# Performance work log

Measured on AMD Instinct MI355X. Metric: run time of the kernel, lower is better.

## Reference

```python
import jax, jax.numpy as jnp
import numpy as np

EPS = 1e-10


def setup_inputs() -> dict:
    key = jax.random.key(0)
    ks = jax.random.split(key, 8)
    N, C, H, W = 32, 512, 14, 14
    D, HID = 2048, 256
    s1 = 1.0 / np.sqrt(C + D)
    s2 = 1.0 / np.sqrt(HID)
    return {
        "local_feature": jax.random.normal(ks[0], (N, C, H, W), jnp.float32),
        "global_feature": jax.random.normal(ks[1], (N, D, 1, 1), jnp.float32),
        "W1": jax.random.normal(ks[2], (C + D, HID), jnp.float32) * s1,
        "b1": jnp.zeros((HID,), jnp.float32),
        "W2": jax.random.normal(ks[3], (HID, HID), jnp.float32) * s2,
        "b2": jnp.zeros((HID,), jnp.float32),
        "W3": jax.random.normal(ks[4], (HID, 1), jnp.float32) * s2,
        "b3": jnp.zeros((1,), jnp.float32),
    }


def reference(local_feature, global_feature, W1, b1, W2, b2, W3, b3):
    # Vectorized form of DMIEstimator.calculate_mi (the per-sample Python loop
    # collapsed into one batched pass with a block-diagonal negative mask).
    N, C, H, W = local_feature.shape
    hw = H * W
    nhw = N * hw
    D = global_feature.shape[1]

    lf = jnp.transpose(local_feature, (0, 2, 3, 1)).reshape(nhw, C)   # [nhw, C]
    gf = global_feature[:, :, 0, 0]                                   # [N, D]

    # combined = cat([global, local], -1); split the first Linear accordingly
    # so the [N*nhw, C+D] concat tensor is never materialized.
    h_loc = lf @ W1[D:]                        # [nhw, HID]
    h_glb = gf @ W1[:D] + b1                   # [N, HID]
    h1 = jax.nn.relu(h_glb[:, None, :] + h_loc[None, :, :])  # [N, nhw, HID]
    h2 = jax.nn.relu(h1 @ W2 + b2)                            # [N, nhw, HID]
    scores = (h2 @ W3)[..., 0] + b3[0]                        # [N, nhw]

    mx = jnp.max(scores, axis=1, keepdims=True)               # [N, 1]
    ex = jnp.exp(scores - mx)

    # negatives for sample i exclude its own hw block [hw*i, hw*(i+1))
    own = (jnp.arange(nhw)[None, :] // hw) == jnp.arange(N)[:, None]  # [N, nhw]
    neg_mean = jnp.where(own, 0.0, ex).sum(axis=1) / (nhw - hw) + EPS  # [N]

    # positive (diagonal) block of scores: scores[i, hw*i : hw*(i+1)]
    pos = scores.reshape(N, N, hw)[jnp.arange(N), jnp.arange(N)]       # [N, hw]

    mi = pos - mx - jnp.log(neg_mean)[:, None]                         # [N, hw]
    return mi.reshape(N, H, W)
```

## Files before the change

### kernel.cpp

```cpp
#include <hip/hip_runtime.h>
#include <math.h>

#define NB   32
#define CC   512
#define DD   2048
#define HWP  196
#define NHW  6272
#define HID  256

typedef _Float16 h8 __attribute__((ext_vector_type(8)));
typedef _Float16 h4 __attribute__((ext_vector_type(4)));
typedef float    f4 __attribute__((ext_vector_type(4)));
union F4H8 { f4 f; h8 h; };

__device__ __forceinline__ int fragIdx(int j, int k) {
    return ((j >> 6) << 14) + (((k >> 5) * 4 + ((j & 63) >> 4)) << 9)
         + (((((k >> 3) & 3) << 4) + (j & 15)) << 3) + (k & 7);
}

__global__ __launch_bounds__(256) void prep_kernel(const float* __restrict__ lf,
                                                   const float* __restrict__ gf,
                                                   const float* __restrict__ W1,
                                                   const float* __restrict__ W2,
                                                   float* __restrict__ hpart,
                                                   _Float16* __restrict__ W2F,
                                                   _Float16* __restrict__ W1F,
                                                   _Float16* __restrict__ lf16T) {
    int bid = blockIdx.x, tid = threadIdx.x;
    if (bid < 512) {
        int i = bid >> 4, ky = bid & 15, k = tid;
        const float* g = gf + (size_t)i * DD + ky * 128;
        const float* w = W1 + (size_t)(ky * 128) * HID + k;
        float a0 = 0.f, a1 = 0.f, a2 = 0.f, a3 = 0.f;
        #pragma unroll 8
        for (int r = 0; r < 128; r += 4) {
            a0 = fmaf(g[r + 0], w[(size_t)(r + 0) * HID], a0);
            a1 = fmaf(g[r + 1], w[(size_t)(r + 1) * HID], a1);
            a2 = fmaf(g[r + 2], w[(size_t)(r + 2) * HID], a2);
            a3 = fmaf(g[r + 3], w[(size_t)(r + 3) * HID], a3);
        }
        hpart[((size_t)i * 16 + ky) * HID + k] = (a0 + a1) + (a2 + a3);
    } else if (bid < 608) {
        int tg = (bid - 512) * 256 + tid;
        if (tg < 8192) {
            int t = tg, F = t >> 6, l = t & 63;
            int k2t = F >> 3, ks = F & 7;
            int kb = ks * 32 + (l >> 4) * 8;
            int n  = k2t * 16 + (l & 15);
            _Float16* o = W2F + (size_t)t * 8;
            #pragma unroll
            for (int j = 0; j < 8; j++) o[j] = (_Float16)W2[(size_t)(kb + j) * HID + n];
        } else {
            int t = tg - 8192, F = t >> 6, l = t & 63;
            int k2t = F >> 4, ks = F & 15;
            int kb = ks * 32 + (l >> 4) * 8;
            int n  = k2t * 16 + (l & 15);
            const float* W1c = W1 + (size_t)DD * HID;
            _Float16* o = W1F + (size_t)t * 8;
            #pragma unroll
            for (int j = 0; j < 8; j++) o[j] = (_Float16)W1c[(size_t)(kb + j) * HID + n];
        }
    } else {
        __shared__ _Float16 sT[64][HWP + 4];
        int b = bid - 608;
        int n = b >> 3, c0 = (b & 7) * 64;
        for (int task = tid; task < 64 * 49; task += 256) {
            int c = task / 49, f = task - c * 49;
            f4 v = *(const f4*)&lf[((size_t)n * CC + c0 + c) * HWP + f * 4];
            h4 o = { (_Float16)v.x, (_Float16)v.y, (_Float16)v.z, (_Float16)v.w };
            *(h4*)&sT[c][f * 4] = o;
        }
        __syncthreads();
        for (int task = tid; task < 8 * HWP; task += 256) {
            int ch = task / HWP, p = task - ch * HWP;
            h8 o;
            #pragma unroll
            for (int cc = 0; cc < 8; cc++) o[cc] = sT[ch * 8 + cc][p];
            *(h8*)&lf16T[((size_t)(n * HWP + p)) * CC + c0 + ch * 8] = o;
        }
    }
}

__global__ __launch_bounds__(256, 2) void hlocF_kernel(const _Float16* __restrict__ lf16T,
                                                       const _Float16* __restrict__ W1F,
                                                       const float* __restrict__ hpart,
                                                       const float* __restrict__ b1,
                                                       _Float16* __restrict__ g16,
                                                       _Float16* __restrict__ hF) {
    if (blockIdx.x == 196) {
        int kh = blockIdx.y;
        for (int x = threadIdx.x; x < 16 * HID; x += 256) {
            int i = kh * 16 + (x >> 8), k = x & 255;
            float s = b1[k];
            #pragma unroll
            for (int ky = 0; ky < 16; ky++) s += hpart[((size_t)i * 16 + ky) * HID + k];
            g16[(size_t)i * HID + k] = (_Float16)s;
        }
        return;
    }
    __shared__ _Float16 sLf[32][CC + 16];
    int tid = threadIdx.x;
    int w = tid >> 6, l = tid & 63, quad = l >> 4, ln = l & 15;
    int j0 = blockIdx.x * 32;
    int khalf = blockIdx.y;

    #pragma unroll
    for (int s = 0; s < 8; s++) {
        int y = s * 256 + tid;
        int row = y >> 6, col = (y & 63) * 8;
        h8 v = *(const h8*)&lf16T[(size_t)(j0 + row) * CC + col];
        *(h8*)&sLf[row][col] = v;
    }

    F4H8 Af[32];
    {
        const f4* src = (const f4*)W1F + l;
        #pragma unroll
        for (int mt = 0; mt < 2; mt++)
            #pragma unroll
            for (int ks = 0; ks < 16; ks++)
                Af[mt * 16 + ks].f = src[(size_t)((khalf * 8 + w * 2 + mt) * 16 + ks) * 64];
    }
    __syncthreads();

    f4 acc[4] = {};
    #pragma unroll
    for (int ks = 0; ks < 16; ks++) {
        h8 bF[2];
        #pragma unroll
        for (int nt = 0; nt < 2; nt++)
            bF[nt] = *(const h8*)&sLf[nt * 16 + ln][ks * 32 + quad * 8];
        #pragma unroll
        for (int mt = 0; mt < 2; mt++)
            #pragma unroll
            for (int nt = 0; nt < 2; nt++)
                acc[mt * 2 + nt] = __builtin_amdgcn_mfma_f32_16x16x32_f16(Af[mt * 16 + ks].h, bF[nt], acc[mt * 2 + nt], 0, 0, 0);
    }

    #pragma unroll
    for (int mt = 0; mt < 2; mt++)
        #pragma unroll
        for (int nt = 0; nt < 2; nt++)
            #pragma unroll
            for (int r = 0; r < 4; r++) {
                int j  = j0 + nt * 16 + ln;
                int k2 = khalf * 128 + w * 32 + mt * 16 + quad * 4 + r;
                hF[fragIdx(j, k2)] = (_Float16)acc[mt * 2 + nt][r];
            }
}

__global__ __launch_bounds__(512, 4) void score_kernel(const _Float16* __restrict__ hF,
                                                       const _Float16* __restrict__ g16,
                                                       const _Float16* __restrict__ W2F,
                                                       const float* __restrict__ b2,
                                                       const float* __restrict__ W3,
                                                       const float* __restrict__ b3,
                                                       float* __restrict__ scores) {
    __shared__ _Float16 sA[128 * HID];
    __shared__ float sRed[128][12];
    int tid = threadIdx.x, w = tid >> 6, l = tid & 63, quad = l >> 4, ln = l & 15;
    int bid = blockIdx.x;
    int i = bid & 31, jt = bid >> 5;

    F4H8 Af[16];
    {
        const f4* src = (const f4*)W2F + l;
        #pragma unroll
        for (int mt = 0; mt < 2; mt++)
            #pragma unroll
            for (int ks = 0; ks < 8; ks++)
                Af[mt * 8 + ks].f = src[(size_t)((w * 2 + mt) * 8 + ks) * 64];
    }
    const _Float16* gbase = g16 + (size_t)i * HID;
    float bias3 = b3[0];

    {
        const _Float16* hbase = hF + (size_t)(jt * 2) * 16384;
        h8 z = {};
        #pragma unroll
        for (int s = 0; s < 8; s++) {
            int y  = s * 512 + tid;
            int y2 = y & 2047;
            h8 hv = *(const h8*)&hbase[y * 8];
            h8 gq = *(const h8*)&gbase[(y2 >> 8) * 32 + ((y2 >> 4) & 3) * 8];
            *(h8*)&sA[y * 8] = __builtin_elementwise_max(hv + gq, z);
        }
    }
    __syncthreads();

    #pragma unroll 1
    for (int pass = 0; pass < 4; pass++) {
        f4 acc[4];
        #pragma unroll
        for (int mt = 0; mt < 2; mt++) {
            f4 bv = *(const f4*)&b2[w * 32 + mt * 16 + quad * 4];
            #pragma unroll
            for (int nt = 0; nt < 2; nt++) acc[mt * 2 + nt] = bv;
        }
        #pragma unroll
        for (int ks = 0; ks < 8; ks++) {
            #pragma unroll
            for (int nt = 0; nt < 2; nt++) {
                int ntg = pass * 2 + nt;
                int base = (ntg >= 4) ? 16384 + (ks * 4 + (ntg - 4)) * 512
                                      : (ks * 4 + ntg) * 512;
                h8 hz = *(const h8*)&sA[base + l * 8];
                #pragma unroll
                for (int mt = 0; mt < 2; mt++)
                    acc[mt * 2 + nt] = __builtin_amdgcn_mfma_f32_16x16x32_f16(Af[mt * 8 + ks].h, hz, acc[mt * 2 + nt], 0, 0, 0);
            }
        }
        #pragma unroll
        for (int nt = 0; nt < 2; nt++) {
            float s = 0.f;
            #pragma unroll
            for (int mt = 0; mt < 2; mt++) {
                f4 w3v = *(const f4*)&W3[w * 32 + mt * 16 + quad * 4];
                s += fmaxf(acc[mt * 2 + nt][0], 0.f) * w3v.x
                   + fmaxf(acc[mt * 2 + nt][1], 0.f) * w3v.y
                   + fmaxf(acc[mt * 2 + nt][2], 0.f) * w3v.z
                   + fmaxf(acc[mt * 2 + nt][3], 0.f) * w3v.w;
            }
            s += __shfl_xor(s, 16, 64);
            s += __shfl_xor(s, 32, 64);
            if (quad == 0) sRed[(pass * 2 + nt) * 16 + ln][w] = s;
        }
    }
    __syncthreads();
    if (tid < 128) {
        f4 a = *(const f4*)&sRed[tid][0];
        f4 b = *(const f4*)&sRed[tid][4];
        scores[(size_t)i * NHW + jt * 128 + tid] =
            a.x + a.y + a.z + a.w + b.x + b.y + b.z + b.w + bias3;
    }
}

__global__ __launch_bounds__(1024) void reduce_kernel(const float* __restrict__ scores,
                                                      float* __restrict__ out) {
    int i = blockIdx.x, tid = threadIdx.x;
    const float* row = scores + (size_t)i * NHW;
    const f4* row4 = (const f4*)row;
    __shared__ float sW[16], sW2[16], sval[2];
    float mx = -1e30f;
    for (int q = tid; q < 1568; q += 1024) {
        f4 v = row4[q];
        mx = fmaxf(mx, fmaxf(fmaxf(v.x, v.y), fmaxf(v.z, v.w)));
    }
    #pragma unroll
    for (int off = 32; off > 0; off >>= 1) mx = fmaxf(mx, __shfl_down(mx, off, 64));
    if ((tid & 63) == 0) sW[tid >> 6] = mx;
    __syncthreads();
    if (tid == 0) {
        float m = sW[0];
        for (int c = 1; c < 16; c++) m = fmaxf(m, sW[c]);
        sval[0] = m;
    }
    __syncthreads();
    mx = sval[0];
    int q0 = i * 49, q1 = q0 + 49;
    float tot = 0.f, ownv = 0.f;
    for (int q = tid; q < 1568; q += 1024) {
        f4 v = row4[q];
        float e = expf(v.x - mx) + expf(v.y - mx) + expf(v.z - mx) + expf(v.w - mx);
        tot += e;
        if (q >= q0 && q < q1) ownv += e;
    }
    #pragma unroll
    for (int off = 32; off > 0; off >>= 1) {
        tot  += __shfl_down(tot, off, 64);
        ownv += __shfl_down(ownv, off, 64);
    }
    if ((tid & 63) == 0) { sW[tid >> 6] = tot; sW2[tid >> 6] = ownv; }
    __syncthreads();
    if (tid == 0) {
        float t = 0.f, o = 0.f;
        for (int c = 0; c < 16; c++) { t += sW[c]; o += sW2[c]; }
        float neg_mean = (t - o) / (float)(NHW - HWP) + 1e-10f;
        sval[1] = mx + logf(neg_mean);
    }
    __syncthreads();
    float sub = sval[1];
    if (tid < HWP) out[(size_t)i * HWP + tid] = row[i * HWP + tid] - sub;
}

extern "C" void kernel_launch(void* const* d_in, const int* in_sizes, int n_in,
                              void* d_out, int out_size, void* d_ws, size_t ws_size,
                              hipStream_t stream) {
    const float* lf = (const float*)d_in[0];
    const float* gf = (const float*)d_in[1];
    const float* W1 = (const float*)d_in[2];
    const float* b1 = (const float*)d_in[3];
    const float* W2 = (const float*)d_in[4];
    const float* b2 = (const float*)d_in[5];
    const float* W3 = (const float*)d_in[6];
    const float* b3 = (const float*)d_in[7];
    float* out = (float*)d_out;

    char* ws = (char*)d_ws;
    _Float16* hF     = (_Float16*)ws;
    _Float16* g16    = (_Float16*)(ws + 3211264);
    _Float16* W2F    = (_Float16*)(ws + 3227648);
    _Float16* W1F    = (_Float16*)(ws + 3358720);
    _Float16* lf16T  = (_Float16*)(ws + 3620864);
    float*    scores = (float*)   (ws + 10043392);
    float*    hpart  = (float*)   (ws + 10846208);

    hipLaunchKernelGGL(prep_kernel, dim3(864), dim3(256), 0, stream,
                       lf, gf, W1, W2, hpart, W2F, W1F, lf16T);
    hipLaunchKernelGGL(hlocF_kernel, dim3(197, 2), dim3(256), 0, stream,
                       lf16T, W1F, hpart, b1, g16, hF);
    hipLaunchKernelGGL(score_kernel, dim3(1568), dim3(512), 0, stream,
                       hF, g16, W2F, b2, W3, b3, scores);
    hipLaunchKernelGGL(reduce_kernel, dim3(NB), dim3(1024), 0, stream, scores, out);
}
```

Baseline: 122.7 us.

## Move W2 fragment conversion into hlocF and give each block all output columns

The W2-to-fp16 fragment conversion moves from the prep kernel into spare blocks of the hlocF kernel. hlocF is restructured from a 197x2 grid of 256-thread blocks, each covering half the hidden columns, into 214 blocks of 512 threads. Each block now loads its 32-row local-feature tile into shared memory once and computes all 256 output columns in two passes, which halves the redundant tile loads. The register footprint per wave also shrinks, but each block now does serial passes and there are fewer blocks in total.

After: 134.7 us. +9.8%, slower.

```diff
diff --git a/kernel.cpp b/kernel.cpp
--- a/kernel.cpp
+++ b/kernel.cpp
@@ -21,9 +21,7 @@
 __global__ __launch_bounds__(256) void prep_kernel(const float* __restrict__ lf,
                                                    const float* __restrict__ gf,
                                                    const float* __restrict__ W1,
-                                                   const float* __restrict__ W2,
                                                    float* __restrict__ hpart,
-                                                   _Float16* __restrict__ W2F,
                                                    _Float16* __restrict__ W1F,
                                                    _Float16* __restrict__ lf16T) {
     int bid = blockIdx.x, tid = threadIdx.x;
@@ -40,29 +38,19 @@
             a3 = fmaf(g[r + 3], w[(size_t)(r + 3) * HID], a3);
         }
         hpart[((size_t)i * 16 + ky) * HID + k] = (a0 + a1) + (a2 + a3);
-    } else if (bid < 608) {
-        int tg = (bid - 512) * 256 + tid;
-        if (tg < 8192) {
-            int t = tg, F = t >> 6, l = t & 63;
-            int k2t = F >> 3, ks = F & 7;
-            int kb = ks * 32 + (l >> 4) * 8;
-            int n  = k2t * 16 + (l & 15);
-            _Float16* o = W2F + (size_t)t * 8;
-            #pragma unroll
-            for (int j = 0; j < 8; j++) o[j] = (_Float16)W2[(size_t)(kb + j) * HID + n];
-        } else {
-            int t = tg - 8192, F = t >> 6, l = t & 63;
-            int k2t = F >> 4, ks = F & 15;
-            int kb = ks * 32 + (l >> 4) * 8;
-            int n  = k2t * 16 + (l & 15);
-            const float* W1c = W1 + (size_t)DD * HID;
-            _Float16* o = W1F + (size_t)t * 8;
-            #pragma unroll
-            for (int j = 0; j < 8; j++) o[j] = (_Float16)W1c[(size_t)(kb + j) * HID + n];
-        }
+    } else if (bid < 576) {
+        int t = (bid - 512) * 256 + tid;
+        int F = t >> 6, l = t & 63;
+        int k2t = F >> 4, ks = F & 15;
+        int kb = ks * 32 + (l >> 4) * 8;
+        int n  = k2t * 16 + (l & 15);
+        const float* W1c = W1 + (size_t)DD * HID;
+        _Float16* o = W1F + (size_t)t * 8;
+        #pragma unroll
+        for (int j = 0; j < 8; j++) o[j] = (_Float16)W1c[(size_t)(kb + j) * HID + n];
     } else {
         __shared__ _Float16 sT[64][HWP + 4];
-        int b = bid - 608;
+        int b = bid - 576;
         int n = b >> 3, c0 = (b & 7) * 64;
         for (int task = tid; task < 64 * 49; task += 256) {
             int c = task / 49, f = task - c * 49;
@@ -81,72 +69,79 @@
     }
 }
 
-__global__ __launch_bounds__(256, 2) void hlocF_kernel(const _Float16* __restrict__ lf16T,
+__global__ __launch_bounds__(512, 4) void hlocF_kernel(const _Float16* __restrict__ lf16T,
                                                        const _Float16* __restrict__ W1F,
                                                        const float* __restrict__ hpart,
                                                        const float* __restrict__ b1,
+                                                       const float* __restrict__ W2,
                                                        _Float16* __restrict__ g16,
+                                                       _Float16* __restrict__ W2F,
                                                        _Float16* __restrict__ hF) {
-    if (blockIdx.x == 196) {
-        int kh = blockIdx.y;
-        for (int x = threadIdx.x; x < 16 * HID; x += 256) {
-            int i = kh * 16 + (x >> 8), k = x & 255;
-            float s = b1[k];
-            #pragma unroll
-            for (int ky = 0; ky < 16; ky++) s += hpart[((size_t)i * 16 + ky) * HID + k];
-            g16[(size_t)i * HID + k] = (_Float16)s;
+    int bid = blockIdx.x, tid = threadIdx.x;
+    if (bid >= 196) {
+        if (bid < 198) {
+            int kh = bid - 196;
+            for (int x = tid; x < 16 * HID; x += 512) {
+                int i = kh * 16 + (x >> 8), k = x & 255;
+                float s = b1[k];
+                #pragma unroll
+                for (int ky = 0; ky < 16; ky++) s += hpart[((size_t)i * 16 + ky) * HID + k];
+                g16[(size_t)i * HID + k] = (_Float16)s;
+            }
+        } else {
+            int t = (bid - 198) * 512 + tid;
+            if (t < 8192) {
+                int F = t >> 6, l = t & 63;
+                int k2t = F >> 3, ks = F & 7;
+                int kb = ks * 32 + (l >> 4) * 8;
+                int n  = k2t * 16 + (l & 15);
+                _Float16* o = W2F + (size_t)t * 8;
+                #pragma unroll
+                for (int j = 0; j < 8; j++) o[j] = (_Float16)W2[(size_t)(kb + j) * HID + n];
+            }
         }
         return;
     }
+
     __shared__ _Float16 sLf[32][CC + 16];
-    int tid = threadIdx.x;
     int w = tid >> 6, l = tid & 63, quad = l >> 4, ln = l & 15;
-    int j0 = blockIdx.x * 32;
-    int khalf = blockIdx.y;
+    int j0 = bid * 32;
 
     #pragma unroll
-    for (int s = 0; s < 8; s++) {
-        int y = s * 256 + tid;
+    for (int s = 0; s < 4; s++) {
+        int y = s * 512 + tid;
         int row = y >> 6, col = (y & 63) * 8;
-        h8 v = *(const h8*)&lf16T[(size_t)(j0 + row) * CC + col];
-        *(h8*)&sLf[row][col] = v;
-    }
-
-    F4H8 Af[32];
-    {
-        const f4* src = (const f4*)W1F + l;
-        #pragma unroll
-        for (int mt = 0; mt < 2; mt++)
-            #pragma unroll
-            for (int ks = 0; ks < 16; ks++)
-                Af[mt * 16 + ks].f = src[(size_t)((khalf * 8 + w * 2 + mt) * 16 + ks) * 64];
-    }
-    __syncthreads();
-
-    f4 acc[4] = {};
-    #pragma unroll
-    for (int ks = 0; ks < 16; ks++) {
-        h8 bF[2];
-        #pragma unroll
-        for (int nt = 0; nt < 2; nt++)
-            bF[nt] = *(const h8*)&sLf[nt * 16 + ln][ks * 32 + quad * 8];
-        #pragma unroll
-        for (int mt = 0; mt < 2; mt++)
-            #pragma unroll
-            for (int nt = 0; nt < 2; nt++)
-                acc[mt * 2 + nt] = __builtin_amdgcn_mfma_f32_16x16x32_f16(Af[mt * 16 + ks].h, bF[nt], acc[mt * 2 + nt], 0, 0, 0);
-    }
-
-    #pragma unroll
-    for (int mt = 0; mt < 2; mt++)
+        *(h8*)&sLf[row][col] = *(const h8*)&lf16T[(size_t)(j0 + row) * CC + col];
+    }
+    __syncthreads();
+
+    const f4* src = (const f4*)W1F + l;
+    #pragma unroll 1
+    for (int pass = 0; pass < 2; pass++) {
+        int k2t = pass * 8 + w;
+        F4H8 Af[16];
+        #pragma unroll
+        for (int ks = 0; ks < 16; ks++)
+            Af[ks].f = src[(size_t)(k2t * 16 + ks) * 64];
+
+        f4 acc[2] = {};
+        #pragma unroll
+        for (int ks = 0; ks < 16; ks++) {
+            #pragma unroll
+            for (int nt = 0; nt < 2; nt++) {
+                h8 bF = *(const h8*)&sLf[nt * 16 + ln][ks * 32 + quad * 8];
+                acc[nt] = __builtin_amdgcn_mfma_f32_16x16x32_f16(Af[ks].h, bF, acc[nt], 0, 0, 0);
+            }
+        }
         #pragma unroll
         for (int nt = 0; nt < 2; nt++)
             #pragma unroll
             for (int r = 0; r < 4; r++) {
                 int j  = j0 + nt * 16 + ln;
-                int k2 = khalf * 128 + w * 32 + mt * 16 + quad * 4 + r;
-                hF[fragIdx(j, k2)] = (_Float16)acc[mt * 2 + nt][r];
-            }
+                int k2 = k2t * 16 + quad * 4 + r;
+                hF[fragIdx(j, k2)] = (_Float16)acc[nt][r];
+            }
+    }
 }
 
 __global__ __launch_bounds__(512, 4) void score_kernel(const _Float16* __restrict__ hF,
@@ -305,10 +300,10 @@
     float*    scores = (float*)   (ws + 10043392);
     float*    hpart  = (float*)   (ws + 10846208);
 
-    hipLaunchKernelGGL(prep_kernel, dim3(864), dim3(256), 0, stream,
-                       lf, gf, W1, W2, hpart, W2F, W1F, lf16T);
-    hipLaunchKernelGGL(hlocF_kernel, dim3(197, 2), dim3(256), 0, stream,
-                       lf16T, W1F, hpart, b1, g16, hF);
+    hipLaunchKernelGGL(prep_kernel, dim3(832), dim3(256), 0, stream,
+                       lf, gf, W1, hpart, W1F, lf16T);
+    hipLaunchKernelGGL(hlocF_kernel, dim3(214), dim3(512), 0, stream,
+                       lf16T, W1F, hpart, b1, W2, g16, W2F, hF);
     hipLaunchKernelGGL(score_kernel, dim3(1568), dim3(512), 0, stream,
                        hF, g16, W2F, b2, W3, b3, scores);
     hipLaunchKernelGGL(reduce_kernel, dim3(NB), dim3(1024), 0, stream, scores, out);
```
